# Kernel tuning notes

Hardware: AMD Instinct MI355X
Metric: run time of the kernel (lower is better)

The kernel has to match this reference:

```python
import jax, jax.numpy as jnp
import numpy as np

B, T, H, DK, DV, HID, C = 2, 4096, 16, 128, 128, 2048, 64  # chunk size 64 (fla default)
EPS = 1e-5


def setup_inputs() -> dict:
    key = jax.random.key(0)
    ks = jax.random.split(key, 8)
    s = 0.02
    return dict(
        hidden_ab=jax.random.normal(ks[0], (B, T, HID), jnp.float32),
        hidden_g=jax.random.normal(ks[1], (B, T, HID), jnp.float32),
        q=jax.random.normal(ks[2], (B, T, H, DK), jnp.float32),
        k=jax.random.normal(ks[3], (B, T, H, DK), jnp.float32),
        v=jax.random.normal(ks[4], (B, T, H, DV), jnp.float32),
        Wb=jax.random.normal(ks[5], (HID, H), jnp.float32) * s,
        Wg=jax.random.normal(ks[6], (HID, H), jnp.float32) * s,
        o_norm_w=jnp.ones((DV,), jnp.float32),
        o_proj_w=jax.random.normal(ks[7], (H, DV, DK), jnp.float32) * s,
    )


def _l2norm(x):
    return x * jax.lax.rsqrt(jnp.sum(x * x, -1, keepdims=True) + 1e-6)


def reference(hidden_ab, hidden_g, q, k, v, Wb, Wg, o_norm_w, o_proj_w):
    # beta gate per head (training path: sigmoid(b_proj(hidden_ab)))
    beta = jax.nn.sigmoid(hidden_ab @ Wb)  # [B,T,H]
    # qk_norm == 'l2' -> l2 normalization inside the kernel, q scaled by dk^-0.5
    q = _l2norm(q)
    k = _l2norm(k)
    scale = DK ** -0.5
    N = T // C

    def toc(x, d):  # [B,T,H,d] -> [N,B,H,C,d]
        return x.reshape(B, N, C, H, d).transpose(1, 0, 3, 2, 4)

    qc = toc(q * scale, DK)
    kc = toc(k, DK)
    vc = toc(v, DV)
    bc = beta.reshape(B, N, C, H).transpose(1, 0, 3, 2)  # [N,B,H,C]

    k_beta = kc * bc[..., None]
    v_beta = vc * bc[..., None]

    # intra-chunk UT transform: Tm = (I + strict_lower(k_beta k^T))^{-1}
    Lm = jnp.tril(jnp.einsum('nbhik,nbhjk->nbhij', k_beta, kc), -1)  # [N,B,H,C,C]
    eye = jnp.eye(C, dtype=q.dtype)
    Tm = jax.scipy.linalg.solve_triangular(eye + Lm, jnp.broadcast_to(eye, Lm.shape), lower=True)
    u = Tm @ v_beta   # [N,B,H,C,DV]
    w = Tm @ k_beta   # [N,B,H,C,DK]
    attn = jnp.tril(jnp.einsum('nbhik,nbhjk->nbhij', qc, kc))  # causal intra-chunk scores

    def step(S, ins):  # S: [B,H,DK,DV] carried state
        qn, kn, an, un, wn = ins
        vi = un - wn @ S                                   # corrected values
        on = qn @ S + an @ vi                              # inter + intra chunk output
        S = S + jnp.einsum('bhck,bhcv->bhkv', kn, vi)      # state update
        return S, on

    S0 = jnp.zeros((B, H, DK, DV), q.dtype)
    _, o = jax.lax.scan(step, S0, (qc, kc, attn, u, w))    # o: [N,B,H,C,DV]
    o = o.transpose(1, 0, 3, 2, 4).reshape(B, T, H, DV)

    # FusedRMSNormSwishGate with per-head scalar gate broadcast over DV
    g = hidden_g @ Wg  # [B,T,H]
    o = o * jax.lax.rsqrt(jnp.mean(o * o, -1, keepdims=True) + EPS) * o_norm_w
    o = o * (g * jax.nn.sigmoid(g))[..., None]

    # GroupLinear: per-head DV -> head_dim projection, then flatten heads
    out = jnp.einsum('bthv,hvd->bthd', o, o_proj_w).reshape(B, T, H * DK)
    return out
```

## Files before the change

### kernel.cpp

```cpp
#include <hip/hip_runtime.h>
#include <hip/hip_bf16.h>

#define BB 2
#define TT 4096
#define HH 16
#define DKk 128
#define DVv 128
#define HIDD 2048
#define CC 64
#define NN 64
#define GG 8
#define QSCALE 0.08838834764831845f

static __device__ __forceinline__ unsigned short f2bf(float f) {
  unsigned u = __float_as_uint(f);
  u += 0x7fffu + ((u >> 16) & 1u);
  return (unsigned short)(u >> 16);
}
static __device__ __forceinline__ float bf2f(unsigned short s) {
  return __uint_as_float(((unsigned)s) << 16);
}

static __device__ __forceinline__ void barrier_lds_only() {
  asm volatile("s_waitcnt lgkmcnt(0)\n\ts_barrier" ::: "memory");
}

typedef short bf8 __attribute__((ext_vector_type(8)));
typedef float f4 __attribute__((ext_vector_type(4)));

__global__ __launch_bounds__(256) void k0_wt(
    const float* __restrict__ Wb, const float* __restrict__ Wg,
    unsigned short* __restrict__ Wtb, unsigned short* __restrict__ Wtg) {
  int blk = blockIdx.x;
  const float* W = (blk < 8) ? Wb : Wg;
  unsigned short* Wt = (blk < 8) ? Wtb : Wtg;
  int k0 = (blk & 7) * 256;
  int tid = threadIdx.x;
  __shared__ unsigned short st[16][272];
  const float* p = W + (size_t)(k0 + tid) * HH;
#pragma unroll
  for (int h4 = 0; h4 < 4; h4++) {
    float4 x = *(const float4*)(p + h4 * 4);
    st[h4 * 4 + 0][tid] = f2bf(x.x);
    st[h4 * 4 + 1][tid] = f2bf(x.y);
    st[h4 * 4 + 2][tid] = f2bf(x.z);
    st[h4 * 4 + 3][tid] = f2bf(x.w);
  }
  __syncthreads();
  int h = tid >> 4, c = (tid & 15) << 4;
#pragma unroll
  for (int j = 0; j < 16; j++)
    Wt[(size_t)h * HIDD + k0 + c + j] = st[h][c + j];
}

__global__ __launch_bounds__(256) void k1_beta_g(
    const float* __restrict__ hab, const float* __restrict__ hg,
    const unsigned short* __restrict__ Wtb, const unsigned short* __restrict__ Wtg,
    float* __restrict__ beta, float* __restrict__ graw) {
  int tile = blockIdx.x;
  int tid = threadIdx.x;
  int w = tid >> 6, lane = tid & 63;
  int proj = w >> 1, ks = w & 1;
  int n16 = lane & 15, qd = lane >> 4;
  const float* hid = proj ? hg : hab;
  const unsigned short* Wt = proj ? Wtg : Wtb;
  size_t rowbase = (size_t)(tile * 16 + n16) * HIDD;
  int k0 = ks * 1024;

  f4 acc = {0.f, 0.f, 0.f, 0.f};
  for (int s = 0; s < 32; s++) {
    int kk = k0 + s * 32 + qd * 8;
    const float* hp = hid + rowbase + kk;
    float4 h0 = *(const float4*)hp;
    float4 h1 = *(const float4*)(hp + 4);
    bf8 a;
    a[0] = (short)f2bf(h0.x); a[1] = (short)f2bf(h0.y);
    a[2] = (short)f2bf(h0.z); a[3] = (short)f2bf(h0.w);
    a[4] = (short)f2bf(h1.x); a[5] = (short)f2bf(h1.y);
    a[6] = (short)f2bf(h1.z); a[7] = (short)f2bf(h1.w);
    bf8 b = *(const bf8*)&Wt[(size_t)n16 * HIDD + kk];
    acc = __builtin_amdgcn_mfma_f32_16x16x32_bf16(a, b, acc, 0, 0, 0);
  }

  __shared__ float red[2][16][17];
  if (ks == 1) {
#pragma unroll
    for (int r = 0; r < 4; r++) red[proj][qd * 4 + r][n16] = acc[r];
  }
  __syncthreads();
  if (ks == 0) {
#pragma unroll
    for (int r = 0; r < 4; r++) {
      float s = acc[r] + red[proj][qd * 4 + r][n16];
      size_t t = (size_t)(tile * 16 + qd * 4 + r) * HH + n16;
      if (proj == 0) beta[t] = 1.f / (1.f + expf(-s));
      else           graw[t] = s;
    }
  }
}

__global__ __launch_bounds__(256) void k2_l2norm(
    const float* __restrict__ q, const float* __restrict__ k,
    unsigned short* __restrict__ qn, unsigned short* __restrict__ kn) {
  int lane = threadIdx.x & 63, wave = threadIdx.x >> 6;
  for (int u = 0; u < 2; u++) {
    int vec = blockIdx.x * 8 + wave * 2 + u;
    size_t off = (size_t)vec * 64 + lane;
    float2 q2 = ((const float2*)q)[off];
    float2 k2 = ((const float2*)k)[off];
    float sq = q2.x * q2.x + q2.y * q2.y;
    float sk = k2.x * k2.x + k2.y * k2.y;
#pragma unroll
    for (int m = 32; m; m >>= 1) { sq += __shfl_xor(sq, m); sk += __shfl_xor(sk, m); }
    float rq = rsqrtf(sq + 1e-6f) * QSCALE;
    float rk = rsqrtf(sk + 1e-6f);
    unsigned pq = (unsigned)f2bf(q2.x * rq) | ((unsigned)f2bf(q2.y * rq) << 16);
    unsigned pk = (unsigned)f2bf(k2.x * rk) | ((unsigned)f2bf(k2.y * rk) << 16);
    ((unsigned*)qn)[off] = pq;
    ((unsigned*)kn)[off] = pk;
  }
}

#define SW 72
#define O_M0R 0
#define O_M0T 4608
#define O_M1R 9216
#define O_M1T 13824
#define O_TB  18432
#define ARENA_SH 23040

__global__ __launch_bounds__(256) void k3_chunk(
    const unsigned short* __restrict__ qn, const unsigned short* __restrict__ kn,
    const float* __restrict__ beta,
    unsigned short* __restrict__ Tg, unsigned short* __restrict__ Ag) {
  int cid = blockIdx.x;
  int n = cid & (NN - 1);
  int bh = cid / NN;
  int h = bh & (HH - 1);
  int b = bh / HH;
  int tid = threadIdx.x;
  int w = tid >> 6;
  int lane = tid & 63;
  int n16 = lane & 15;
  int qd = lane >> 4;
  int r0 = w * 16;

  __shared__ __align__(16) unsigned short arena[ARENA_SH];
  __shared__ float sb[CC];
  unsigned short* sk = arena;
  unsigned short* sq = arena + 8704;

  int t0 = n * CC;
#pragma unroll
  for (int p = 0; p < 4; p++) {
    int id = p * 256 + tid, row = id >> 4, c8 = (id & 15) << 3;
    size_t g = ((size_t)((b * TT + t0 + row) * HH + h)) * DKk + c8;
    *(uint4*)&sk[row * 136 + c8] = *(const uint4*)(kn + g);
    *(uint4*)&sq[row * 136 + c8] = *(const uint4*)(qn + g);
  }
  if (tid < CC) sb[tid] = beta[(size_t)((b * TT + t0 + tid) * HH + h)];
  __syncthreads();

  f4 at[4], mk[4];
#pragma unroll
  for (int ct = 0; ct < 4; ct++) { at[ct] = (f4){0,0,0,0}; mk[ct] = (f4){0,0,0,0}; }
#pragma unroll
  for (int s = 0; s < 4; s++) {
    bf8 aq = *(const bf8*)&sq[(r0 + n16) * 136 + s * 32 + qd * 8];
    bf8 ak = *(const bf8*)&sk[(r0 + n16) * 136 + s * 32 + qd * 8];
#pragma unroll
    for (int ct = 0; ct < 4; ct++) {
      bf8 bk = *(const bf8*)&sk[(ct * 16 + n16) * 136 + s * 32 + qd * 8];
      at[ct] = __builtin_amdgcn_mfma_f32_16x16x32_bf16(aq, bk, at[ct], 0, 0, 0);
      mk[ct] = __builtin_amdgcn_mfma_f32_16x16x32_bf16(ak, bk, mk[ct], 0, 0, 0);
    }
  }

  size_t abase = (size_t)cid * (CC * CC);
  f4 tf[4];
  float mpv[4][4];
#pragma unroll
  for (int ct = 0; ct < 4; ct++) {
#pragma unroll
    for (int r = 0; r < 4; r++) {
      int i = r0 + qd * 4 + r, j = ct * 16 + n16;
      Ag[abase + i * CC + j] = f2bf((j <= i) ? at[ct][r] : 0.f);
      float mp = (j < i) ? -sb[i] * mk[ct][r] : 0.f;
      mpv[ct][r] = mp;
      tf[ct][r] = (i == j) ? 1.f : mp;
    }
  }
  __syncthreads();

#pragma unroll
  for (int ct = 0; ct < 4; ct++) {
#pragma unroll
    for (int r = 0; r < 4; r++) {
      int i = r0 + qd * 4 + r, j = ct * 16 + n16;
      unsigned short hm = f2bf(mpv[ct][r]);
      arena[O_M0R + i * SW + j] = hm;
      arena[O_M0T + j * SW + i] = hm;
      arena[O_TB + j * SW + i] = f2bf(tf[ct][r]);
    }
  }
  __syncthreads();

  int p = 0;
  for (int it = 1; it <= 5; it++) {
    int mrp = p ? O_M1R : O_M0R, mtp = p ? O_M1T : O_M0T;
    int mrn = p ? O_M0R : O_M1R, mtn = p ? O_M0T : O_M1T;
    f4 nr[4];
#pragma unroll
    for (int ct = 0; ct < 4; ct++) nr[ct] = (f4){0,0,0,0};
#pragma unroll
    for (int s = 0; s < 2; s++) {
      bf8 a = *(const bf8*)&arena[mrp + (r0 + n16) * SW + s * 32 + qd * 8];
#pragma unroll
      for (int ct = 0; ct < 4; ct++) {
        bf8 bb = *(const bf8*)&arena[mtp + (ct * 16 + n16) * SW + s * 32 + qd * 8];
        nr[ct] = __builtin_amdgcn_mfma_f32_16x16x32_bf16(a, bb, nr[ct], 0, 0, 0);
      }
    }
#pragma unroll
    for (int ct = 0; ct < 4; ct++) {
#pragma unroll
      for (int r = 0; r < 4; r++) {
        int i = r0 + qd * 4 + r, j = ct * 16 + n16;
        unsigned short hm = f2bf(nr[ct][r]);
        arena[mrn + i * SW + j] = hm;
        arena[mtn + j * SW + i] = hm;
      }
    }
    __syncthreads();

#pragma unroll
    for (int s = 0; s < 2; s++) {
      bf8 a = *(const bf8*)&arena[mrn + (r0 + n16) * SW + s * 32 + qd * 8];
#pragma unroll
      for (int ct = 0; ct < 4; ct++) {
        bf8 bb = *(const bf8*)&arena[O_TB + (ct * 16 + n16) * SW + s * 32 + qd * 8];
        tf[ct] = __builtin_amdgcn_mfma_f32_16x16x32_bf16(a, bb, tf[ct], 0, 0, 0);
      }
    }
    __syncthreads();

    if (it < 5) {
#pragma unroll
      for (int ct = 0; ct < 4; ct++) {
#pragma unroll
        for (int r = 0; r < 4; r++) {
          int i = r0 + qd * 4 + r, j = ct * 16 + n16;
          arena[O_TB + j * SW + i] = f2bf(tf[ct][r]);
        }
      }
    }
    p = 1 - p;
  }

#pragma unroll
  for (int ct = 0; ct < 4; ct++) {
#pragma unroll
    for (int r = 0; r < 4; r++) {
      int i = r0 + qd * 4 + r, j = ct * 16 + n16;
      Tg[abase + i * CC + j] = f2bf(tf[ct][r]);
    }
  }
}

__global__ __launch_bounds__(256) void k4_scan(
    const unsigned short* __restrict__ qn, const unsigned short* __restrict__ kn,
    const float* __restrict__ v, const float* __restrict__ beta,
    const unsigned short* __restrict__ Tg, const unsigned short* __restrict__ Ag,
    float* __restrict__ o) {
  int bi = blockIdx.x;
  int jg = bi >> 5;
  int bh = bi & 31;
  int h = bh & (HH - 1);
  int b = bh >> 4;
  int tid = threadIdx.x;
  int j0 = jg * 16;
  int w = tid >> 6;
  int lane = tid & 63;
  int n16 = lane & 15;
  int qd = lane >> 4;
  int r0 = w * 16;
  int dkbase = w * 32;

  __shared__ __align__(16) unsigned short sk[CC * 136];
  __shared__ __align__(16) unsigned short sq[CC * 136];
  __shared__ __align__(16) unsigned short sT[CC * 72];
  __shared__ __align__(16) unsigned short sA[CC * 72];
  __shared__ __align__(16) unsigned short sSb[16 * 136];
  __shared__ __align__(16) unsigned short sxT[16 * 72];
  __shared__ __align__(16) unsigned short svT[16 * 72];
  __shared__ float sb[CC];

  f4 S0 = {0.f, 0.f, 0.f, 0.f}, S1 = {0.f, 0.f, 0.f, 0.f};
  for (int i = tid; i < 16 * 136; i += 256) sSb[i] = 0;

  int bhBase = (b * HH + h) * NN;

  uint4 pk[4], pq[4], pt[2], pa[2];
  float4 pv;
  float pb = 0.f;

  int rowA = r0 + n16;
  int swzA = ((rowA >> 3) & 7);

  {
#pragma unroll
    for (int p = 0; p < 4; p++) {
      int id = p * 256 + tid, row = id >> 4, c8 = (id & 15) << 3;
      size_t g = ((size_t)((b * TT + row) * HH + h)) * DKk + c8;
      pk[p] = *(const uint4*)(kn + g);
      pq[p] = *(const uint4*)(qn + g);
    }
    size_t cb = (size_t)bhBase * (CC * CC);
#pragma unroll
    for (int p = 0; p < 2; p++) {
      int id = p * 256 + tid, row = id >> 3, c8 = (id & 7) << 3;
      pt[p] = *(const uint4*)(Tg + cb + row * CC + c8);
      pa[p] = *(const uint4*)(Ag + cb + row * CC + c8);
    }
    {
      int c = tid >> 2, c4 = (tid & 3) << 2;
      pv = *(const float4*)(v + ((size_t)((b * TT + c) * HH + h)) * DVv + j0 + c4);
    }
    if (tid < CC) pb = beta[(size_t)((b * TT + tid) * HH + h)];
  }

  for (int n = 0; n < NN; n++) {
    int t0 = n * CC;
#pragma unroll
    for (int p = 0; p < 4; p++) {
      int id = p * 256 + tid, row = id >> 4, g = id & 15;
      int gk = (g ^ ((row >> 3) & 7)) << 3;
      *(uint4*)&sk[row * 136 + gk] = pk[p];
      *(uint4*)&sq[row * 136 + (g << 3)] = pq[p];
    }
#pragma unroll
    for (int p = 0; p < 2; p++) {
      int id = p * 256 + tid, row = id >> 3, c8 = (id & 7) << 3;
      *(uint4*)&sT[row * 72 + c8] = pt[p];
      *(uint4*)&sA[row * 72 + c8] = pa[p];
    }
    {
      int c = tid >> 2, c4 = (tid & 3) << 2;
      sxT[(c4 + 0) * 72 + c] = f2bf(pv.x);
      sxT[(c4 + 1) * 72 + c] = f2bf(pv.y);
      sxT[(c4 + 2) * 72 + c] = f2bf(pv.z);
      sxT[(c4 + 3) * 72 + c] = f2bf(pv.w);
    }
    if (tid < CC) sb[tid] = pb;
    barrier_lds_only();

    if (n + 1 < NN) {
      int t0n = t0 + CC;
#pragma unroll
      for (int p = 0; p < 4; p++) {
        int id = p * 256 + tid, row = id >> 4, c8 = (id & 15) << 3;
        size_t g = ((size_t)((b * TT + t0n + row) * HH + h)) * DKk + c8;
        pk[p] = *(const uint4*)(kn + g);
        pq[p] = *(const uint4*)(qn + g);
      }
      size_t cb = (size_t)(bhBase + n + 1) * (CC * CC);
#pragma unroll
      for (int p = 0; p < 2; p++) {
        int id = p * 256 + tid, row = id >> 3, c8 = (id & 7) << 3;
        pt[p] = *(const uint4*)(Tg + cb + row * CC + c8);
        pa[p] = *(const uint4*)(Ag + cb + row * CC + c8);
      }
      {
        int c = tid >> 2, c4 = (tid & 3) << 2;
        pv = *(const float4*)(v + ((size_t)((b * TT + t0n + c) * HH + h)) * DVv + j0 + c4);
      }
      if (tid < CC) pb = beta[(size_t)((b * TT + t0n + tid) * HH + h)];
    }

    {
      f4 acc = {0.f, 0.f, 0.f, 0.f};
#pragma unroll
      for (int s = 0; s < 4; s++) {
        bf8 a = *(const bf8*)&sk[rowA * 136 + (((s * 4 + qd) ^ swzA) << 3)];
        bf8 bb = *(const bf8*)&sSb[n16 * 136 + s * 32 + qd * 8];
        acc = __builtin_amdgcn_mfma_f32_16x16x32_bf16(a, bb, acc, 0, 0, 0);
      }
#pragma unroll
      for (int r = 0; r < 4; r++) {
        int c = r0 + qd * 4 + r;
        float vval = bf2f(sxT[n16 * 72 + c]);
        sxT[n16 * 72 + c] = f2bf(sb[c] * (vval - acc[r]));
      }
    }
    barrier_lds_only();

    {
      f4 acc = {0.f, 0.f, 0.f, 0.f};
#pragma unroll
      for (int s = 0; s < 2; s++) {
        bf8 a = *(const bf8*)&sT[(r0 + n16) * 72 + s * 32 + qd * 8];
        bf8 bb = *(const bf8*)&sxT[n16 * 72 + s * 32 + qd * 8];
        acc = __builtin_amdgcn_mfma_f32_16x16x32_bf16(a, bb, acc, 0, 0, 0);
      }
#pragma unroll
      for (int r = 0; r < 4; r++) {
        int c = r0 + qd * 4 + r;
        svT[n16 * 72 + c] = f2bf(acc[r]);
      }
    }
    barrier_lds_only();

    {
      f4 acc = {0.f, 0.f, 0.f, 0.f};
#pragma unroll
      for (int s = 0; s < 4; s++) {
        bf8 a = *(const bf8*)&sq[(r0 + n16) * 136 + s * 32 + qd * 8];
        bf8 bb = *(const bf8*)&sSb[n16 * 136 + s * 32 + qd * 8];
        acc = __builtin_amdgcn_mfma_f32_16x16x32_bf16(a, bb, acc, 0, 0, 0);
      }
#pragma unroll
      for (int s = 0; s < 2; s++) {
        bf8 a = *(const bf8*)&sA[(r0 + n16) * 72 + s * 32 + qd * 8];
        bf8 bb = *(const bf8*)&svT[n16 * 72 + s * 32 + qd * 8];
        acc = __builtin_amdgcn_mfma_f32_16x16x32_bf16(a, bb, acc, 0, 0, 0);
      }
#pragma unroll
      for (int r = 0; r < 4; r++) {
        int c = r0 + qd * 4 + r;
        o[((size_t)((b * TT + t0 + c) * HH + h)) * DVv + j0 + n16] = acc[r];
      }
    }

    {
#pragma unroll
      for (int t = 0; t < 2; t++) {
        int dkt = dkbase + t * 16;
        int col = dkt + n16;
        int gg = col >> 3, co = col & 7;
        f4 acc = t ? S1 : S0;
#pragma unroll
        for (int s = 0; s < 2; s++) {
          int sq8 = (s * 4 + qd) & 7;
          bf8 a;
#pragma unroll
          for (int j = 0; j < 8; j++)
            a[j] = (short)sk[(s * 32 + qd * 8 + j) * 136 + (((gg ^ sq8) << 3) | co)];
          bf8 bb = *(const bf8*)&svT[n16 * 72 + s * 32 + qd * 8];
          acc = __builtin_amdgcn_mfma_f32_16x16x32_bf16(a, bb, acc, 0, 0, 0);
        }
        if (t) S1 = acc; else S0 = acc;
      }
    }
    barrier_lds_only();

#pragma unroll
    for (int r = 0; r < 4; r++) {
      sSb[n16 * 136 + dkbase + qd * 4 + r] = f2bf(S0[r]);
      sSb[n16 * 136 + dkbase + 16 + qd * 4 + r] = f2bf(S1[r]);
    }
  }
}

__global__ __launch_bounds__(256) void k5_out(
    const float* __restrict__ graw, const float* __restrict__ onw,
    const float* __restrict__ opw, float* __restrict__ out) {
  int bi = blockIdx.x;
  int h = bi & (HH - 1);
  int tt = (bi >> 4) & 127;
  int b = bi >> 11;
  int t0 = tt * 32;
  int tid = threadIdx.x;

  __shared__ __align__(16) unsigned short sP[DVv * DKk];
  __shared__ __align__(16) float so[32 * 129];
  __shared__ float smul[32];
  __shared__ float snw[DVv];

  const float* P = opw + (size_t)h * DVv * DKk;
  for (int r = 0; r < 16; r++) {
    int idx4 = r * 256 + tid;
    float4 pvv = *(const float4*)(P + ((size_t)idx4 << 2));
    unsigned p0 = (unsigned)f2bf(pvv.x) | ((unsigned)f2bf(pvv.y) << 16);
    unsigned p1 = (unsigned)f2bf(pvv.z) | ((unsigned)f2bf(pvv.w) << 16);
    *(uint2*)&sP[idx4 << 2] = make_uint2(p0, p1);
  }
  for (int r = 0; r < 16; r++) {
    int idx = r * 256 + tid;
    int t = idx >> 7, d = idx & 127;
    so[t * 129 + d] = out[((size_t)((b * TT + t0 + t) * HH + h)) * DVv + d];
  }
  if (tid < DVv) snw[tid] = onw[tid];
  __syncthreads();

  {
    int t = tid >> 3, l8 = tid & 7;
    float ss = 0.f;
    for (int j = 0; j < 16; j++) { float x = so[t * 129 + l8 + (j << 3)]; ss += x * x; }
    ss += __shfl_down(ss, 4, 8);
    ss += __shfl_down(ss, 2, 8);
    ss += __shfl_down(ss, 1, 8);
    if (l8 == 0) {
      float rms = rsqrtf(ss * (1.f / 128.f) + 1e-5f);
      float gv = graw[(size_t)((b * TT + t0 + t) * HH + h)];
      float sig = 1.f / (1.f + expf(-gv));
      smul[t] = rms * gv * sig;
    }
  }
  __syncthreads();
  for (int r = 0; r < 16; r++) {
    int idx = r * 256 + tid;
    int t = idx >> 7, d = idx & 127;
    so[t * 129 + d] *= smul[t] * snw[d];
  }
  __syncthreads();

  {
    int ttile = tid >> 5;
    int dt = tid & 31;
    int tb = ttile << 2;
    int d0 = dt << 2;
    float acc[4][4];
#pragma unroll
    for (int a = 0; a < 4; a++)
#pragma unroll
      for (int e = 0; e < 4; e++) acc[a][e] = 0.f;
    for (int vv = 0; vv < DVv; vv++) {
      uint2 u = *(const uint2*)&sP[vv * DKk + d0];
      float p0 = __uint_as_float(u.x << 16);
      float p1 = __uint_as_float(u.x & 0xffff0000u);
      float p2 = __uint_as_float(u.y << 16);
      float p3 = __uint_as_float(u.y & 0xffff0000u);
#pragma unroll
      for (int a = 0; a < 4; a++) {
        float ov = so[(tb + a) * 129 + vv];
        acc[a][0] += ov * p0; acc[a][1] += ov * p1; acc[a][2] += ov * p2; acc[a][3] += ov * p3;
      }
    }
#pragma unroll
    for (int a = 0; a < 4; a++) {
      size_t go = ((size_t)((b * TT + t0 + tb + a) * HH + h)) * DKk + d0;
      float4 r; r.x = acc[a][0]; r.y = acc[a][1]; r.z = acc[a][2]; r.w = acc[a][3];
      *(float4*)(out + go) = r;
    }
  }
}

extern "C" void kernel_launch(void* const* d_in, const int* in_sizes, int n_in,
                              void* d_out, int out_size, void* d_ws, size_t ws_size,
                              hipStream_t stream) {
  (void)in_sizes; (void)n_in; (void)out_size; (void)ws_size;
  const float* hab = (const float*)d_in[0];
  const float* hg  = (const float*)d_in[1];
  const float* q   = (const float*)d_in[2];
  const float* k   = (const float*)d_in[3];
  const float* v   = (const float*)d_in[4];
  const float* Wb  = (const float*)d_in[5];
  const float* Wg  = (const float*)d_in[6];
  const float* onw = (const float*)d_in[7];
  const float* opw = (const float*)d_in[8];
  float* out = (float*)d_out;

  char* ws = (char*)d_ws;
  float* beta          = (float*)(ws);
  float* graw          = (float*)(ws + 524288);
  unsigned short* qn   = (unsigned short*)(ws + 1048576);
  unsigned short* kn   = (unsigned short*)(ws + 34603008);
  unsigned short* Tg   = (unsigned short*)(ws + 68157440);
  unsigned short* Ag   = (unsigned short*)(ws + 84934656);
  unsigned short* Wtb  = (unsigned short*)(ws + 101711872);
  unsigned short* Wtg  = (unsigned short*)(ws + 101777408);

  hipLaunchKernelGGL(k0_wt, dim3(16), dim3(256), 0, stream,
                     Wb, Wg, Wtb, Wtg);
  hipLaunchKernelGGL(k1_beta_g, dim3(TT * BB / 16), dim3(256), 0, stream,
                     hab, hg, Wtb, Wtg, beta, graw);
  hipLaunchKernelGGL(k2_l2norm, dim3(BB * TT * HH / 8), dim3(256), 0, stream,
                     q, k, qn, kn);
  hipLaunchKernelGGL(k3_chunk, dim3(BB * HH * NN), dim3(256), 0, stream,
                     qn, kn, beta, Tg, Ag);
  hipLaunchKernelGGL(k4_scan, dim3(BB * HH * GG), dim3(256), 0, stream,
                     qn, kn, v, beta, Tg, Ag, out);
  hipLaunchKernelGGL(k5_out, dim3(BB * (TT / 32) * HH), dim3(256), 0, stream,
                     graw, onw, opw, out);
}
```

Before: 643.2 us.

## Precompute A·T and k^T·T per chunk to shorten the sequential scan

The chunk kernel now multiplies the causal score matrix by the UT inverse (A·T) and the transposed keys by the inverse (k^T·T) with MFMA, and writes these products to global memory in place of A and T. The scan kernel can then apply the correction directly. It computes x = beta*(v - kS), then o = qS + (A·T)x and S += (k^T·T)x, which removes one dependent matmul stage and one barrier from each serial chunk step. It also double-buffers the per-chunk LDS tiles and issues the q·S and k·S MFMAs together. The cost is more global traffic (a 128x64 k^T·T tile per chunk) plus extra MFMA work in the parallel chunk kernel, and rounding intermediates to bf16 changes numerics slightly.

```diff
diff --git a/kernel.cpp b/kernel.cpp
--- a/kernel.cpp
+++ b/kernel.cpp
@@ -122,17 +122,17 @@
 }
 
 #define SW 72
-#define O_M0R 0
-#define O_M0T 4608
-#define O_M1R 9216
-#define O_M1T 13824
-#define O_TB  18432
-#define ARENA_SH 23040
+#define K3_M0R 8704
+#define K3_M0T 13312
+#define K3_M1R 17920
+#define K3_M1T 22528
+#define K3_TB  27136
+#define K3_ARENA 31744
 
 __global__ __launch_bounds__(256) void k3_chunk(
     const unsigned short* __restrict__ qn, const unsigned short* __restrict__ kn,
     const float* __restrict__ beta,
-    unsigned short* __restrict__ Tg, unsigned short* __restrict__ Ag) {
+    unsigned short* __restrict__ ATg, unsigned short* __restrict__ Ktg) {
   int cid = blockIdx.x;
   int n = cid & (NN - 1);
   int bh = cid / NN;
@@ -145,7 +145,7 @@
   int qd = lane >> 4;
   int r0 = w * 16;
 
-  __shared__ __align__(16) unsigned short arena[ARENA_SH];
+  __shared__ __align__(16) unsigned short arena[K3_ARENA];
   __shared__ float sb[CC];
   unsigned short* sk = arena;
   unsigned short* sq = arena + 8704;
@@ -176,7 +176,6 @@
     }
   }
 
-  size_t abase = (size_t)cid * (CC * CC);
   f4 tf[4];
   float mpv[4][4];
 #pragma unroll
@@ -184,7 +183,7 @@
 #pragma unroll
     for (int r = 0; r < 4; r++) {
       int i = r0 + qd * 4 + r, j = ct * 16 + n16;
-      Ag[abase + i * CC + j] = f2bf((j <= i) ? at[ct][r] : 0.f);
+      at[ct][r] = (j <= i) ? at[ct][r] : 0.f;
       float mp = (j < i) ? -sb[i] * mk[ct][r] : 0.f;
       mpv[ct][r] = mp;
       tf[ct][r] = (i == j) ? 1.f : mp;
@@ -198,17 +197,17 @@
     for (int r = 0; r < 4; r++) {
       int i = r0 + qd * 4 + r, j = ct * 16 + n16;
       unsigned short hm = f2bf(mpv[ct][r]);
-      arena[O_M0R + i * SW + j] = hm;
-      arena[O_M0T + j * SW + i] = hm;
-      arena[O_TB + j * SW + i] = f2bf(tf[ct][r]);
+      arena[K3_M0R + i * SW + j] = hm;
+      arena[K3_M0T + j * SW + i] = hm;
+      arena[K3_TB + j * SW + i] = f2bf(tf[ct][r]);
     }
   }
   __syncthreads();
 
   int p = 0;
   for (int it = 1; it <= 5; it++) {
-    int mrp = p ? O_M1R : O_M0R, mtp = p ? O_M1T : O_M0T;
-    int mrn = p ? O_M0R : O_M1R, mtn = p ? O_M0T : O_M1T;
+    int mrp = p ? K3_M1R : K3_M0R, mtp = p ? K3_M1T : K3_M0T;
+    int mrn = p ? K3_M0R : K3_M1R, mtn = p ? K3_M0T : K3_M1T;
     f4 nr[4];
 #pragma unroll
     for (int ct = 0; ct < 4; ct++) nr[ct] = (f4){0,0,0,0};
@@ -238,7 +237,7 @@
       bf8 a = *(const bf8*)&arena[mrn + (r0 + n16) * SW + s * 32 + qd * 8];
 #pragma unroll
       for (int ct = 0; ct < 4; ct++) {
-        bf8 bb = *(const bf8*)&arena[O_TB + (ct * 16 + n16) * SW + s * 32 + qd * 8];
+        bf8 bb = *(const bf8*)&arena[K3_TB + (ct * 16 + n16) * SW + s * 32 + qd * 8];
         tf[ct] = __builtin_amdgcn_mfma_f32_16x16x32_bf16(a, bb, tf[ct], 0, 0, 0);
       }
     }
@@ -250,7 +249,7 @@
 #pragma unroll
         for (int r = 0; r < 4; r++) {
           int i = r0 + qd * 4 + r, j = ct * 16 + n16;
-          arena[O_TB + j * SW + i] = f2bf(tf[ct][r]);
+          arena[K3_TB + j * SW + i] = f2bf(tf[ct][r]);
         }
       }
     }
@@ -262,7 +261,58 @@
 #pragma unroll
     for (int r = 0; r < 4; r++) {
       int i = r0 + qd * 4 + r, j = ct * 16 + n16;
-      Tg[abase + i * CC + j] = f2bf(tf[ct][r]);
+      arena[K3_M0R + i * SW + j] = f2bf(at[ct][r]);
+      arena[K3_TB + j * SW + i] = f2bf(tf[ct][r]);
+    }
+  }
+  __syncthreads();
+
+  {
+    f4 ac[4];
+#pragma unroll
+    for (int ct = 0; ct < 4; ct++) ac[ct] = (f4){0,0,0,0};
+#pragma unroll
+    for (int s = 0; s < 2; s++) {
+      bf8 a = *(const bf8*)&arena[K3_M0R + (r0 + n16) * SW + s * 32 + qd * 8];
+#pragma unroll
+      for (int ct = 0; ct < 4; ct++) {
+        bf8 bb = *(const bf8*)&arena[K3_TB + (ct * 16 + n16) * SW + s * 32 + qd * 8];
+        ac[ct] = __builtin_amdgcn_mfma_f32_16x16x32_bf16(a, bb, ac[ct], 0, 0, 0);
+      }
+    }
+    size_t abase = (size_t)cid * (CC * CC);
+#pragma unroll
+    for (int ct = 0; ct < 4; ct++)
+#pragma unroll
+      for (int r = 0; r < 4; r++)
+        ATg[abase + (r0 + qd * 4 + r) * CC + ct * 16 + n16] = f2bf(ac[ct][r]);
+  }
+
+  {
+    size_t kbase = (size_t)cid * (DKk * CC);
+#pragma unroll
+    for (int t = 0; t < 2; t++) {
+      int dkt = w * 32 + t * 16;
+      f4 ac[4];
+#pragma unroll
+      for (int ct = 0; ct < 4; ct++) ac[ct] = (f4){0,0,0,0};
+#pragma unroll
+      for (int s = 0; s < 2; s++) {
+        bf8 a;
+#pragma unroll
+        for (int jj = 0; jj < 8; jj++)
+          a[jj] = (short)sk[(s * 32 + qd * 8 + jj) * 136 + dkt + n16];
+#pragma unroll
+        for (int ct = 0; ct < 4; ct++) {
+          bf8 bb = *(const bf8*)&arena[K3_TB + (ct * 16 + n16) * SW + s * 32 + qd * 8];
+          ac[ct] = __builtin_amdgcn_mfma_f32_16x16x32_bf16(a, bb, ac[ct], 0, 0, 0);
+        }
+      }
+#pragma unroll
+      for (int ct = 0; ct < 4; ct++)
+#pragma unroll
+        for (int r = 0; r < 4; r++)
+          Ktg[kbase + (dkt + qd * 4 + r) * CC + ct * 16 + n16] = f2bf(ac[ct][r]);
     }
   }
 }
@@ -270,7 +320,7 @@
 __global__ __launch_bounds__(256) void k4_scan(
     const unsigned short* __restrict__ qn, const unsigned short* __restrict__ kn,
     const float* __restrict__ v, const float* __restrict__ beta,
-    const unsigned short* __restrict__ Tg, const unsigned short* __restrict__ Ag,
+    const unsigned short* __restrict__ ATg, const unsigned short* __restrict__ Ktg,
     float* __restrict__ o) {
   int bi = blockIdx.x;
   int jg = bi >> 5;
@@ -288,11 +338,10 @@
 
   __shared__ __align__(16) unsigned short sk[CC * 136];
   __shared__ __align__(16) unsigned short sq[CC * 136];
-  __shared__ __align__(16) unsigned short sT[CC * 72];
-  __shared__ __align__(16) unsigned short sA[CC * 72];
   __shared__ __align__(16) unsigned short sSb[16 * 136];
-  __shared__ __align__(16) unsigned short sxT[16 * 72];
-  __shared__ __align__(16) unsigned short svT[16 * 72];
+  __shared__ __align__(16) unsigned short sAT[2][CC * SW];
+  __shared__ __align__(16) unsigned short sKt[2][DKk * SW];
+  __shared__ __align__(16) unsigned short sxT[2][16 * SW];
   __shared__ float sb[CC];
 
   f4 S0 = {0.f, 0.f, 0.f, 0.f}, S1 = {0.f, 0.f, 0.f, 0.f};
@@ -300,12 +349,9 @@
 
   int bhBase = (b * HH + h) * NN;
 
-  uint4 pk[4], pq[4], pt[2], pa[2];
+  uint4 pk[4], pq[4], pat[2], pkt[4];
   float4 pv;
   float pb = 0.f;
-
-  int rowA = r0 + n16;
-  int swzA = ((rowA >> 3) & 7);
 
   {
 #pragma unroll
@@ -319,8 +365,13 @@
 #pragma unroll
     for (int p = 0; p < 2; p++) {
       int id = p * 256 + tid, row = id >> 3, c8 = (id & 7) << 3;
-      pt[p] = *(const uint4*)(Tg + cb + row * CC + c8);
-      pa[p] = *(const uint4*)(Ag + cb + row * CC + c8);
+      pat[p] = *(const uint4*)(ATg + cb + row * CC + c8);
+    }
+    size_t kb = (size_t)bhBase * (DKk * CC);
+#pragma unroll
+    for (int p = 0; p < 4; p++) {
+      int id = p * 256 + tid, row = id >> 3, c8 = (id & 7) << 3;
+      pkt[p] = *(const uint4*)(Ktg + kb + row * CC + c8);
     }
     {
       int c = tid >> 2, c4 = (tid & 3) << 2;
@@ -331,25 +382,32 @@
 
   for (int n = 0; n < NN; n++) {
     int t0 = n * CC;
+    unsigned short* xT = sxT[n & 1];
+    unsigned short* aT = sAT[n & 1];
+    unsigned short* kT = sKt[n & 1];
+
 #pragma unroll
     for (int p = 0; p < 4; p++) {
-      int id = p * 256 + tid, row = id >> 4, g = id & 15;
-      int gk = (g ^ ((row >> 3) & 7)) << 3;
-      *(uint4*)&sk[row * 136 + gk] = pk[p];
-      *(uint4*)&sq[row * 136 + (g << 3)] = pq[p];
+      int id = p * 256 + tid, row = id >> 4, c8 = (id & 15) << 3;
+      *(uint4*)&sk[row * 136 + c8] = pk[p];
+      *(uint4*)&sq[row * 136 + c8] = pq[p];
     }
 #pragma unroll
     for (int p = 0; p < 2; p++) {
       int id = p * 256 + tid, row = id >> 3, c8 = (id & 7) << 3;
-      *(uint4*)&sT[row * 72 + c8] = pt[p];
-      *(uint4*)&sA[row * 72 + c8] = pa[p];
+      *(uint4*)&aT[row * SW + c8] = pat[p];
+    }
+#pragma unroll
+    for (int p = 0; p < 4; p++) {
+      int id = p * 256 + tid, row = id >> 3, c8 = (id & 7) << 3;
+      *(uint4*)&kT[row * SW + c8] = pkt[p];
     }
     {
       int c = tid >> 2, c4 = (tid & 3) << 2;
-      sxT[(c4 + 0) * 72 + c] = f2bf(pv.x);
-      sxT[(c4 + 1) * 72 + c] = f2bf(pv.y);
-      sxT[(c4 + 2) * 72 + c] = f2bf(pv.z);
-      sxT[(c4 + 3) * 72 + c] = f2bf(pv.w);
+      xT[(c4 + 0) * SW + c] = f2bf(pv.x);
+      xT[(c4 + 1) * SW + c] = f2bf(pv.y);
+      xT[(c4 + 2) * SW + c] = f2bf(pv.z);
+      xT[(c4 + 3) * SW + c] = f2bf(pv.w);
     }
     if (tid < CC) sb[tid] = pb;
     barrier_lds_only();
@@ -367,8 +425,13 @@
 #pragma unroll
       for (int p = 0; p < 2; p++) {
         int id = p * 256 + tid, row = id >> 3, c8 = (id & 7) << 3;
-        pt[p] = *(const uint4*)(Tg + cb + row * CC + c8);
-        pa[p] = *(const uint4*)(Ag + cb + row * CC + c8);
+        pat[p] = *(const uint4*)(ATg + cb + row * CC + c8);
+      }
+      size_t kb = (size_t)(bhBase + n + 1) * (DKk * CC);
+#pragma unroll
+      for (int p = 0; p < 4; p++) {
+        int id = p * 256 + tid, row = id >> 3, c8 = (id & 7) << 3;
+        pkt[p] = *(const uint4*)(Ktg + kb + row * CC + c8);
       }
       {
         int c = tid >> 2, c4 = (tid & 3) << 2;
@@ -377,86 +440,65 @@
       if (tid < CC) pb = beta[(size_t)((b * TT + t0n + tid) * HH + h)];
     }
 
+    f4 oacc;
     {
-      f4 acc = {0.f, 0.f, 0.f, 0.f};
-#pragma unroll
-      for (int s = 0; s < 4; s++) {
-        bf8 a = *(const bf8*)&sk[rowA * 136 + (((s * 4 + qd) ^ swzA) << 3)];
-        bf8 bb = *(const bf8*)&sSb[n16 * 136 + s * 32 + qd * 8];
-        acc = __builtin_amdgcn_mfma_f32_16x16x32_bf16(a, bb, acc, 0, 0, 0);
-      }
+      bf8 bS0 = *(const bf8*)&sSb[n16 * 136 + 0 * 32 + qd * 8];
+      bf8 bS1 = *(const bf8*)&sSb[n16 * 136 + 1 * 32 + qd * 8];
+      bf8 bS2 = *(const bf8*)&sSb[n16 * 136 + 2 * 32 + qd * 8];
+      bf8 bS3 = *(const bf8*)&sSb[n16 * 136 + 3 * 32 + qd * 8];
+      bf8 aK0 = *(const bf8*)&sk[(r0 + n16) * 136 + 0 * 32 + qd * 8];
+      bf8 aK1 = *(const bf8*)&sk[(r0 + n16) * 136 + 1 * 32 + qd * 8];
+      bf8 aK2 = *(const bf8*)&sk[(r0 + n16) * 136 + 2 * 32 + qd * 8];
+      bf8 aK3 = *(const bf8*)&sk[(r0 + n16) * 136 + 3 * 32 + qd * 8];
+      bf8 aQ0 = *(const bf8*)&sq[(r0 + n16) * 136 + 0 * 32 + qd * 8];
+      bf8 aQ1 = *(const bf8*)&sq[(r0 + n16) * 136 + 1 * 32 + qd * 8];
+      bf8 aQ2 = *(const bf8*)&sq[(r0 + n16) * 136 + 2 * 32 + qd * 8];
+      bf8 aQ3 = *(const bf8*)&sq[(r0 + n16) * 136 + 3 * 32 + qd * 8];
+      f4 xa = {0.f, 0.f, 0.f, 0.f}, xc = {0.f, 0.f, 0.f, 0.f};
+      f4 oa = {0.f, 0.f, 0.f, 0.f}, ob = {0.f, 0.f, 0.f, 0.f};
+      xa = __builtin_amdgcn_mfma_f32_16x16x32_bf16(aK0, bS0, xa, 0, 0, 0);
+      xa = __builtin_amdgcn_mfma_f32_16x16x32_bf16(aK1, bS1, xa, 0, 0, 0);
+      xc = __builtin_amdgcn_mfma_f32_16x16x32_bf16(aK2, bS2, xc, 0, 0, 0);
+      xc = __builtin_amdgcn_mfma_f32_16x16x32_bf16(aK3, bS3, xc, 0, 0, 0);
+      oa = __builtin_amdgcn_mfma_f32_16x16x32_bf16(aQ0, bS0, oa, 0, 0, 0);
+      oa = __builtin_amdgcn_mfma_f32_16x16x32_bf16(aQ1, bS1, oa, 0, 0, 0);
+      ob = __builtin_amdgcn_mfma_f32_16x16x32_bf16(aQ2, bS2, ob, 0, 0, 0);
+      ob = __builtin_amdgcn_mfma_f32_16x16x32_bf16(aQ3, bS3, ob, 0, 0, 0);
+      oacc = oa + ob;
 #pragma unroll
       for (int r = 0; r < 4; r++) {
         int c = r0 + qd * 4 + r;
-        float vval = bf2f(sxT[n16 * 72 + c]);
-        sxT[n16 * 72 + c] = f2bf(sb[c] * (vval - acc[r]));
+        float vv = bf2f(xT[n16 * SW + c]);
+        xT[n16 * SW + c] = f2bf(sb[c] * (vv - (xa[r] + xc[r])));
       }
     }
     barrier_lds_only();
 
     {
-      f4 acc = {0.f, 0.f, 0.f, 0.f};
-#pragma unroll
-      for (int s = 0; s < 2; s++) {
-        bf8 a = *(const bf8*)&sT[(r0 + n16) * 72 + s * 32 + qd * 8];
-        bf8 bb = *(const bf8*)&sxT[n16 * 72 + s * 32 + qd * 8];
-        acc = __builtin_amdgcn_mfma_f32_16x16x32_bf16(a, bb, acc, 0, 0, 0);
-      }
+      bf8 bx0 = *(const bf8*)&xT[n16 * SW + 0 * 32 + qd * 8];
+      bf8 bx1 = *(const bf8*)&xT[n16 * SW + 1 * 32 + qd * 8];
+      bf8 aA0 = *(const bf8*)&aT[(r0 + n16) * SW + 0 * 32 + qd * 8];
+      bf8 aA1 = *(const bf8*)&aT[(r0 + n16) * SW + 1 * 32 + qd * 8];
+      oacc = __builtin_amdgcn_mfma_f32_16x16x32_bf16(aA0, bx0, oacc, 0, 0, 0);
+      oacc = __builtin_amdgcn_mfma_f32_16x16x32_bf16(aA1, bx1, oacc, 0, 0, 0);
 #pragma unroll
       for (int r = 0; r < 4; r++) {
         int c = r0 + qd * 4 + r;
-        svT[n16 * 72 + c] = f2bf(acc[r]);
-      }
-    }
-    barrier_lds_only();
-
-    {
-      f4 acc = {0.f, 0.f, 0.f, 0.f};
-#pragma unroll
-      for (int s = 0; s < 4; s++) {
-        bf8 a = *(const bf8*)&sq[(r0 + n16) * 136 + s * 32 + qd * 8];
-        bf8 bb = *(const bf8*)&sSb[n16 * 136 + s * 32 + qd * 8];
-        acc = __builtin_amdgcn_mfma_f32_16x16x32_bf16(a, bb, acc, 0, 0, 0);
-      }
-#pragma unroll
-      for (int s = 0; s < 2; s++) {
-        bf8 a = *(const bf8*)&sA[(r0 + n16) * 72 + s * 32 + qd * 8];
-        bf8 bb = *(const bf8*)&svT[n16 * 72 + s * 32 + qd * 8];
-        acc = __builtin_amdgcn_mfma_f32_16x16x32_bf16(a, bb, acc, 0, 0, 0);
-      }
+        o[((size_t)((b * TT + t0 + c) * HH + h)) * DVv + j0 + n16] = oacc[r];
+      }
+      bf8 aT0 = *(const bf8*)&kT[(dkbase + n16) * SW + 0 * 32 + qd * 8];
+      bf8 aT1 = *(const bf8*)&kT[(dkbase + n16) * SW + 1 * 32 + qd * 8];
+      S0 = __builtin_amdgcn_mfma_f32_16x16x32_bf16(aT0, bx0, S0, 0, 0, 0);
+      S0 = __builtin_amdgcn_mfma_f32_16x16x32_bf16(aT1, bx1, S0, 0, 0, 0);
+      bf8 aT2 = *(const bf8*)&kT[(dkbase + 16 + n16) * SW + 0 * 32 + qd * 8];
+      bf8 aT3 = *(const bf8*)&kT[(dkbase + 16 + n16) * SW + 1 * 32 + qd * 8];
+      S1 = __builtin_amdgcn_mfma_f32_16x16x32_bf16(aT2, bx0, S1, 0, 0, 0);
+      S1 = __builtin_amdgcn_mfma_f32_16x16x32_bf16(aT3, bx1, S1, 0, 0, 0);
 #pragma unroll
       for (int r = 0; r < 4; r++) {
-        int c = r0 + qd * 4 + r;
-        o[((size_t)((b * TT + t0 + c) * HH + h)) * DVv + j0 + n16] = acc[r];
-      }
-    }
-
-    {
-#pragma unroll
-      for (int t = 0; t < 2; t++) {
-        int dkt = dkbase + t * 16;
-        int col = dkt + n16;
-        int gg = col >> 3, co = col & 7;
-        f4 acc = t ? S1 : S0;
-#pragma unroll
-        for (int s = 0; s < 2; s++) {
-          int sq8 = (s * 4 + qd) & 7;
-          bf8 a;
-#pragma unroll
-          for (int j = 0; j < 8; j++)
-            a[j] = (short)sk[(s * 32 + qd * 8 + j) * 136 + (((gg ^ sq8) << 3) | co)];
-          bf8 bb = *(const bf8*)&svT[n16 * 72 + s * 32 + qd * 8];
-          acc = __builtin_amdgcn_mfma_f32_16x16x32_bf16(a, bb, acc, 0, 0, 0);
-        }
-        if (t) S1 = acc; else S0 = acc;
-      }
-    }
-    barrier_lds_only();
-
-#pragma unroll
-    for (int r = 0; r < 4; r++) {
-      sSb[n16 * 136 + dkbase + qd * 4 + r] = f2bf(S0[r]);
-      sSb[n16 * 136 + dkbase + 16 + qd * 4 + r] = f2bf(S1[r]);
+        sSb[n16 * 136 + dkbase + qd * 4 + r] = f2bf(S0[r]);
+        sSb[n16 * 136 + dkbase + 16 + qd * 4 + r] = f2bf(S1[r]);
+      }
     }
   }
 }
@@ -565,10 +607,10 @@
   float* graw          = (float*)(ws + 524288);
   unsigned short* qn   = (unsigned short*)(ws + 1048576);
   unsigned short* kn   = (unsigned short*)(ws + 34603008);
-  unsigned short* Tg   = (unsigned short*)(ws + 68157440);
-  unsigned short* Ag   = (unsigned short*)(ws + 84934656);
-  unsigned short* Wtb  = (unsigned short*)(ws + 101711872);
-  unsigned short* Wtg  = (unsigned short*)(ws + 101777408);
+  unsigned short* ATg  = (unsigned short*)(ws + 68157440);
+  unsigned short* Ktg  = (unsigned short*)(ws + 84934656);
+  unsigned short* Wtb  = (unsigned short*)(ws + 118489088);
+  unsigned short* Wtg  = (unsigned short*)(ws + 118554624);
 
   hipLaunchKernelGGL(k0_wt, dim3(16), dim3(256), 0, stream,
                      Wb, Wg, Wtb, Wtg);
@@ -577,9 +619,9 @@
   hipLaunchKernelGGL(k2_l2norm, dim3(BB * TT * HH / 8), dim3(256), 0, stream,
                      q, k, qn, kn);
   hipLaunchKernelGGL(k3_chunk, dim3(BB * HH * NN), dim3(256), 0, stream,
-                     qn, kn, beta, Tg, Ag);
+                     qn, kn, beta, ATg, Ktg);
   hipLaunchKernelGGL(k4_scan, dim3(BB * HH * GG), dim3(256), 0, stream,
-                     qn, kn, v, beta, Tg, Ag, out);
+                     qn, kn, v, beta, ATg, Ktg, out);
   hipLaunchKernelGGL(k5_out, dim3(BB * (TT / 32) * HH), dim3(256), 0, stream,
                      graw, onw, opw, out);
 }
```

Result: faster. 611.0 us (-5.0%).
